# Performance work log

Measured on AMD Instinct MI355X. Metric: run time of the kernel, lower is better.

Reference implementation:

```python
import jax, jax.numpy as jnp
import numpy as np

EMBED = 128
NUM_HOPS = 3
VOCAB = 32000
MEM = 50
PAD = 0


def pos_weights(J, d):
    # MemN2N position encoding: 1 - (j+1)/J - (k+1)/d * (1 - 2*(j+1)/J)
    j = jnp.arange(J, dtype=jnp.float32)[:, None]
    k = jnp.arange(d, dtype=jnp.float32)[None, :]
    return 1.0 - (j + 1.0) / J - (k + 1.0) / d * (1.0 - 2.0 * (j + 1.0) / J)


def setup_inputs() -> dict:
    key = jax.random.key(0)
    ks = jax.random.split(key, 10)
    ctx_query = jax.random.randint(ks[0], (16, 10, 20), 0, VOCAB)
    story = jax.random.randint(ks[1], (16, MEM, 40), 0, VOCAB)

    def emb(k):
        w = 0.1 * jax.random.normal(k, (VOCAB, EMBED), dtype=jnp.float32)
        return w.at[PAD].set(0.0)  # padding_idx row is zero

    A_w = emb(ks[2])
    C_w = emb(ks[3])
    B_w = emb(ks[4])
    H_w = 0.1 * jax.random.normal(ks[5], (EMBED, EMBED), dtype=jnp.float32)
    H_b = 0.1 * jax.random.normal(ks[6], (EMBED,), dtype=jnp.float32)
    out_w = 0.1 * jax.random.normal(ks[7], (VOCAB, EMBED), dtype=jnp.float32)
    TA = 0.1 * jax.random.normal(ks[8], (MEM, EMBED), dtype=jnp.float32)
    TC = 0.1 * jax.random.normal(ks[9], (MEM, EMBED), dtype=jnp.float32)
    return {"ctx_query": ctx_query, "story": story, "A_w": A_w, "C_w": C_w,
            "B_w": B_w, "H_w": H_w, "H_b": H_b, "out_w": out_w, "TA": TA, "TC": TC}


def reference(ctx_query, story, A_w, C_w, B_w, H_w, H_b, out_w, TA, TC):
    B, NQ, S = ctx_query.shape
    R, S2 = story.shape[1], story.shape[2]
    cq = ctx_query.reshape(B * NQ, S)
    # story repeated across num_qa (broadcast instead of materialized repeat)
    st = jnp.broadcast_to(story[:, None], (B, NQ, R, S2)).reshape(B * NQ, R, S2)

    qw = pos_weights(S, EMBED)            # [S, d]
    state = jnp.sum(B_w[cq] * qw, axis=1)  # [BN, d]

    sw = pos_weights(S2, EMBED)           # [S2, d]
    for _ in range(NUM_HOPS):             # use_lw=True: A/C tied across hops
        mem = jnp.sum(A_w[st] * sw, axis=2) + TA    # [BN, R, d]
        outm = jnp.sum(C_w[st] * sw, axis=2) + TC   # [BN, R, d]
        probs = jax.nn.softmax(jnp.einsum('brd,bd->br', mem, state), axis=-1)
        response = jnp.einsum('br,brd->bd', probs, outm)  # [BN, d]
        state = response @ H_w.T + H_b + state      # H(response) + state
    return state @ out_w.T                          # [BN, vocab]
```

## Files before the change

kernel.cpp:

```cpp
#include <hip/hip_runtime.h>
#include <hip/hip_bf16.h>
#include <math.h>

#define EMBED 128
#define VOCAB 32000
#define MEMN  50
#define BATCH 16
#define NQ    10
#define SQ    20
#define SS    40
#define BN    (BATCH*NQ)
#define NHOPS 3
#define NV    64

typedef short v8s __attribute__((ext_vector_type(8)));
typedef float v4f __attribute__((ext_vector_type(4)));

__device__ __forceinline__ float posw(int j, int J, int k) {
    float jf = (float)(j + 1) / (float)J;
    return 1.0f - jf - ((float)(k + 1) / (float)EMBED) * (1.0f - 2.0f * jf);
}

__device__ __forceinline__ short f2bf(float f) {
    __hip_bfloat16 h = __float2bfloat16(f);
    return *(short*)&h;
}

__global__ void k_embed(const int* __restrict__ cq, const int* __restrict__ story,
                        const float* __restrict__ Bw, const float* __restrict__ Aw,
                        const float* __restrict__ Cw, const float* __restrict__ TA,
                        const float* __restrict__ TC, const float* __restrict__ Hw,
                        float* __restrict__ state, float* __restrict__ memb,
                        float* __restrict__ outb, float* __restrict__ HwT) {
    int blk = blockIdx.x;
    int t = threadIdx.x;
    if (blk < BN) {
        float acc = 0.f;
        #pragma unroll
        for (int s = 0; s < SQ; ++s) {
            int tok = cq[blk * SQ + s];
            acc += Bw[tok * EMBED + t] * posw(s, SQ, t);
        }
        state[blk * EMBED + t] = acc;
    } else if (blk < BN + BATCH * MEMN) {
        int br = blk - BN;
        int r = br % MEMN;
        float ma = TA[r * EMBED + t];
        float mc = TC[r * EMBED + t];
        const int* toks = story + br * SS;
        #pragma unroll 4
        for (int s = 0; s < SS; ++s) {
            int tok = toks[s];
            float w = posw(s, SS, t);
            ma += Aw[tok * EMBED + t] * w;
            mc += Cw[tok * EMBED + t] * w;
        }
        memb[br * EMBED + t] = ma;
        outb[br * EMBED + t] = mc;
    } else {
        int k = blk - (BN + BATCH * MEMN);
        HwT[k * EMBED + t] = Hw[t * EMBED + k];
    }
}

__global__ void k_hops(const float* __restrict__ memb, const float* __restrict__ outb,
                       const float* __restrict__ HwT, const float* __restrict__ Hb,
                       const float* __restrict__ state, __hip_bfloat16* __restrict__ stateb) {
    __shared__ float lmem[MEMN][EMBED + 1];
    __shared__ float lout[MEMN][EMBED + 1];
    __shared__ float lstate[EMBED];
    __shared__ float lprobs[MEMN];
    __shared__ float lresp[EMBED];
    int bn = blockIdx.x;
    int b  = bn / NQ;
    int t  = threadIdx.x;
    for (int i = t; i < MEMN * EMBED; i += EMBED) {
        int r = i >> 7, d = i & 127;
        lmem[r][d] = memb[b * MEMN * EMBED + i];
        lout[r][d] = outb[b * MEMN * EMBED + i];
    }
    lstate[t] = state[bn * EMBED + t];
    __syncthreads();

    for (int hop = 0; hop < NHOPS; ++hop) {
        float logit = -1e30f;
        if (t < MEMN) {
            float acc = 0.f;
            for (int d = 0; d < EMBED; ++d) acc += lmem[t][d] * lstate[d];
            logit = acc;
        }
        if (t < 64) {
            float m = logit;
            #pragma unroll
            for (int off = 32; off; off >>= 1) m = fmaxf(m, __shfl_xor(m, off, 64));
            float e = (t < MEMN) ? __expf(logit - m) : 0.f;
            float ssum = e;
            #pragma unroll
            for (int off = 32; off; off >>= 1) ssum += __shfl_xor(ssum, off, 64);
            if (t < MEMN) lprobs[t] = e / ssum;
        }
        __syncthreads();
        float resp = 0.f;
        for (int r = 0; r < MEMN; ++r) resp += lprobs[r] * lout[r][t];
        lresp[t] = resp;
        __syncthreads();
        float acc = Hb[t] + lstate[t];
        for (int k = 0; k < EMBED; ++k) acc += lresp[k] * HwT[k * EMBED + t];
        __syncthreads();
        lstate[t] = acc;
        __syncthreads();
    }
    stateb[bn * EMBED + t] = __float2bfloat16(lstate[t]);
}

__global__ __launch_bounds__(256) void k_out(const __hip_bfloat16* __restrict__ stateb,
                                             const float* __restrict__ outw,
                                             float* __restrict__ out) {
    __shared__ __align__(16) __hip_bfloat16 Alds[BN][EMBED + 8];
    __shared__ __align__(16) __hip_bfloat16 Blds[NV][EMBED + 8];
    int t = threadIdx.x;
    int vbase = blockIdx.x * NV;

    #pragma unroll
    for (int i = 0; i < 10; ++i) {
        int e = t + i * 256;
        int row = e >> 4, c8 = (e & 15) << 3;
        *(int4*)&Alds[row][c8] = *(const int4*)&stateb[row * EMBED + c8];
    }
    #pragma unroll
    for (int i = 0; i < 8; ++i) {
        int e = t + i * 256;
        int row = e >> 5, c4 = (e & 31) << 2;
        float4 w = *(const float4*)&outw[(size_t)(vbase + row) * EMBED + c4];
        short4 p;
        p.x = f2bf(w.x); p.y = f2bf(w.y); p.z = f2bf(w.z); p.w = f2bf(w.w);
        *(short4*)&Blds[row][c4] = p;
    }
    __syncthreads();

    int wv = t >> 6;
    int l = t & 63;
    int col16 = l & 15;
    int kg = l >> 4;

    v8s bfrag[4];
    #pragma unroll
    for (int k4 = 0; k4 < 4; ++k4)
        bfrag[k4] = *(v8s*)&Blds[(wv << 4) + col16][k4 * 32 + kg * 8];

    v4f acc[10];
    #pragma unroll
    for (int m = 0; m < 10; ++m) acc[m] = (v4f){0.f, 0.f, 0.f, 0.f};

    #pragma unroll
    for (int k4 = 0; k4 < 4; ++k4) {
        #pragma unroll
        for (int m = 0; m < 10; ++m) {
            v8s af = *(v8s*)&Alds[m * 16 + col16][k4 * 32 + kg * 8];
            acc[m] = __builtin_amdgcn_mfma_f32_16x16x32_bf16(af, bfrag[k4], acc[m], 0, 0, 0);
        }
    }

    int colg = vbase + (wv << 4) + col16;
    #pragma unroll
    for (int m = 0; m < 10; ++m) {
        #pragma unroll
        for (int i = 0; i < 4; ++i) {
            out[(size_t)(m * 16 + kg * 4 + i) * VOCAB + colg] = acc[m][i];
        }
    }
}

extern "C" void kernel_launch(void* const* d_in, const int* in_sizes, int n_in,
                              void* d_out, int out_size, void* d_ws, size_t ws_size,
                              hipStream_t stream) {
    const int*   ctx_query = (const int*)  d_in[0];
    const int*   story     = (const int*)  d_in[1];
    const float* A_w       = (const float*)d_in[2];
    const float* C_w       = (const float*)d_in[3];
    const float* B_w       = (const float*)d_in[4];
    const float* H_w       = (const float*)d_in[5];
    const float* H_b       = (const float*)d_in[6];
    const float* out_w     = (const float*)d_in[7];
    const float* TA        = (const float*)d_in[8];
    const float* TC        = (const float*)d_in[9];
    float* out = (float*)d_out;

    float* ws    = (float*)d_ws;
    float* state = ws;
    float* memb  = state + BN * EMBED;
    float* outb  = memb + BATCH * MEMN * EMBED;
    float* HwT   = outb + BATCH * MEMN * EMBED;
    __hip_bfloat16* stateb = (__hip_bfloat16*)(HwT + EMBED * EMBED);

    k_embed<<<BN + BATCH * MEMN + EMBED, EMBED, 0, stream>>>(
        ctx_query, story, B_w, A_w, C_w, TA, TC, H_w, state, memb, outb, HwT);
    k_hops<<<BN, EMBED, 0, stream>>>(memb, outb, HwT, H_b, state, stateb);
    k_out<<<VOCAB / NV, 256, 0, stream>>>(stateb, out_w, out);
}
```

Before: 35.39 us.

## Restructure embedding gather into float4 loads split across token groups

The embedding kernel now stages token ids in shared memory and has each thread load float4 slices of embedding rows. The 128 threads are split into 4 groups over token positions, and partial sums are reduced through shared memory. Position weights are computed with hoisted per-token coefficients. This aims to raise memory-level parallelism and cut serial dependent gathers per thread, at the cost of extra syncs and a reduction step. The hop kernel loops also get unroll pragmas.

```diff
diff --git a/kernel.cpp b/kernel.cpp
--- a/kernel.cpp
+++ b/kernel.cpp
@@ -16,11 +16,6 @@
 typedef short v8s __attribute__((ext_vector_type(8)));
 typedef float v4f __attribute__((ext_vector_type(4)));
 
-__device__ __forceinline__ float posw(int j, int J, int k) {
-    float jf = (float)(j + 1) / (float)J;
-    return 1.0f - jf - ((float)(k + 1) / (float)EMBED) * (1.0f - 2.0f * jf);
-}
-
 __device__ __forceinline__ short f2bf(float f) {
     __hip_bfloat16 h = __float2bfloat16(f);
     return *(short*)&h;
@@ -32,31 +27,90 @@
                         const float* __restrict__ TC, const float* __restrict__ Hw,
                         float* __restrict__ state, float* __restrict__ memb,
                         float* __restrict__ outb, float* __restrict__ HwT) {
+    __shared__ int ltok[SS];
+    __shared__ float4 redA[4][32];
+    __shared__ float4 redC[4][32];
     int blk = blockIdx.x;
     int t = threadIdx.x;
+    int sg = t >> 5;
+    int d4 = t & 31;
+    int k0 = d4 << 2;
+
     if (blk < BN) {
-        float acc = 0.f;
-        #pragma unroll
-        for (int s = 0; s < SQ; ++s) {
-            int tok = cq[blk * SQ + s];
-            acc += Bw[tok * EMBED + t] * posw(s, SQ, t);
-        }
-        state[blk * EMBED + t] = acc;
+        int bn = blk;
+        if (t < SQ) ltok[t] = cq[bn * SQ + t];
+        __syncthreads();
+        float4 acc = {0.f, 0.f, 0.f, 0.f};
+        #pragma unroll
+        for (int i = 0; i < SQ / 4; ++i) {
+            int s = sg + (i << 2);
+            int tok = ltok[s];
+            float jf = (float)(s + 1) * (1.0f / SQ);
+            float c0 = 1.0f - jf;
+            float c1 = (1.0f - 2.0f * jf) * (1.0f / EMBED);
+            float4 a = *(const float4*)&Bw[(size_t)tok * EMBED + k0];
+            acc.x += a.x * (c0 - (float)(k0 + 1) * c1);
+            acc.y += a.y * (c0 - (float)(k0 + 2) * c1);
+            acc.z += a.z * (c0 - (float)(k0 + 3) * c1);
+            acc.w += a.w * (c0 - (float)(k0 + 4) * c1);
+        }
+        redA[sg][d4] = acc;
+        __syncthreads();
+        if (t < 32) {
+            float4 s0 = redA[0][t], s1 = redA[1][t], s2 = redA[2][t], s3 = redA[3][t];
+            float4 o;
+            o.x = s0.x + s1.x + s2.x + s3.x;
+            o.y = s0.y + s1.y + s2.y + s3.y;
+            o.z = s0.z + s1.z + s2.z + s3.z;
+            o.w = s0.w + s1.w + s2.w + s3.w;
+            *(float4*)&state[bn * EMBED + (t << 2)] = o;
+        }
     } else if (blk < BN + BATCH * MEMN) {
         int br = blk - BN;
         int r = br % MEMN;
-        float ma = TA[r * EMBED + t];
-        float mc = TC[r * EMBED + t];
-        const int* toks = story + br * SS;
-        #pragma unroll 4
-        for (int s = 0; s < SS; ++s) {
-            int tok = toks[s];
-            float w = posw(s, SS, t);
-            ma += Aw[tok * EMBED + t] * w;
-            mc += Cw[tok * EMBED + t] * w;
-        }
-        memb[br * EMBED + t] = ma;
-        outb[br * EMBED + t] = mc;
+        if (t < SS) ltok[t] = story[br * SS + t];
+        __syncthreads();
+        float4 accA = {0.f, 0.f, 0.f, 0.f};
+        float4 accC = {0.f, 0.f, 0.f, 0.f};
+        #pragma unroll
+        for (int i = 0; i < SS / 4; ++i) {
+            int s = sg + (i << 2);
+            int tok = ltok[s];
+            float jf = (float)(s + 1) * (1.0f / SS);
+            float c0 = 1.0f - jf;
+            float c1 = (1.0f - 2.0f * jf) * (1.0f / EMBED);
+            float w0 = c0 - (float)(k0 + 1) * c1;
+            float w1 = c0 - (float)(k0 + 2) * c1;
+            float w2 = c0 - (float)(k0 + 3) * c1;
+            float w3 = c0 - (float)(k0 + 4) * c1;
+            float4 a = *(const float4*)&Aw[(size_t)tok * EMBED + k0];
+            float4 c = *(const float4*)&Cw[(size_t)tok * EMBED + k0];
+            accA.x += a.x * w0; accA.y += a.y * w1; accA.z += a.z * w2; accA.w += a.w * w3;
+            accC.x += c.x * w0; accC.y += c.y * w1; accC.z += c.z * w2; accC.w += c.w * w3;
+        }
+        redA[sg][d4] = accA;
+        redC[sg][d4] = accC;
+        __syncthreads();
+        if (t < 32) {
+            float4 s0 = redA[0][t], s1 = redA[1][t], s2 = redA[2][t], s3 = redA[3][t];
+            float4 ta = *(const float4*)&TA[r * EMBED + (t << 2)];
+            float4 o;
+            o.x = s0.x + s1.x + s2.x + s3.x + ta.x;
+            o.y = s0.y + s1.y + s2.y + s3.y + ta.y;
+            o.z = s0.z + s1.z + s2.z + s3.z + ta.z;
+            o.w = s0.w + s1.w + s2.w + s3.w + ta.w;
+            *(float4*)&memb[br * EMBED + (t << 2)] = o;
+        } else if (t < 64) {
+            int u = t - 32;
+            float4 s0 = redC[0][u], s1 = redC[1][u], s2 = redC[2][u], s3 = redC[3][u];
+            float4 tc = *(const float4*)&TC[r * EMBED + (u << 2)];
+            float4 o;
+            o.x = s0.x + s1.x + s2.x + s3.x + tc.x;
+            o.y = s0.y + s1.y + s2.y + s3.y + tc.y;
+            o.z = s0.z + s1.z + s2.z + s3.z + tc.z;
+            o.w = s0.w + s1.w + s2.w + s3.w + tc.w;
+            *(float4*)&outb[br * EMBED + (u << 2)] = o;
+        }
     } else {
         int k = blk - (BN + BATCH * MEMN);
         HwT[k * EMBED + t] = Hw[t * EMBED + k];
@@ -86,6 +140,7 @@
         float logit = -1e30f;
         if (t < MEMN) {
             float acc = 0.f;
+            #pragma unroll 8
             for (int d = 0; d < EMBED; ++d) acc += lmem[t][d] * lstate[d];
             logit = acc;
         }
@@ -101,10 +156,12 @@
         }
         __syncthreads();
         float resp = 0.f;
+        #pragma unroll 10
         for (int r = 0; r < MEMN; ++r) resp += lprobs[r] * lout[r][t];
         lresp[t] = resp;
         __syncthreads();
         float acc = Hb[t] + lstate[t];
+        #pragma unroll 8
         for (int k = 0; k < EMBED; ++k) acc += lresp[k] * HwT[k * EMBED + t];
         __syncthreads();
         lstate[t] = acc;
@@ -193,7 +250,7 @@
     float* HwT   = outb + BATCH * MEMN * EMBED;
     __hip_bfloat16* stateb = (__hip_bfloat16*)(HwT + EMBED * EMBED);
 
-    k_embed<<<BN + BATCH * MEMN + EMBED, EMBED, 0, stream>>>(
+    k_embed<<<BN + BATCH * MEMN + EMBED, 128, 0, stream>>>(
         ctx_query, story, B_w, A_w, C_w, TA, TC, H_w, state, memb, outb, HwT);
     k_hops<<<BN, EMBED, 0, stream>>>(memb, outb, HwT, H_b, state, stateb);
     k_out<<<VOCAB / NV, 256, 0, stream>>>(stateb, out_w, out);
```

Result: slower. 39.06 us (+10.3%).

## Store state in MFMA fragment layout and drop LDS staging in output GEMM

Applied to the files above, without the earlier changes.

The hop kernel now writes the final bf16 state directly in a fragment-major layout, so the output projection can load MFMA A-operands straight from global memory with contiguous 16-byte loads. The output kernel drops its shared-memory staging and the block barrier. It now runs one 64-thread wave per 16 vocab columns and loads out_w fragments directly into registers. This removes LDS traffic and synchronisation, but it launches four times as many blocks and each wave re-reads the state from L2 rather than sharing it across a block.

```diff
diff --git a/kernel.cpp b/kernel.cpp
--- a/kernel.cpp
+++ b/kernel.cpp
@@ -11,7 +11,6 @@
 #define SS    40
 #define BN    (BATCH*NQ)
 #define NHOPS 3
-#define NV    64
 
 typedef short v8s __attribute__((ext_vector_type(8)));
 typedef float v4f __attribute__((ext_vector_type(4)));
@@ -65,7 +64,7 @@
 
 __global__ void k_hops(const float* __restrict__ memb, const float* __restrict__ outb,
                        const float* __restrict__ HwT, const float* __restrict__ Hb,
-                       const float* __restrict__ state, __hip_bfloat16* __restrict__ stateb) {
+                       const float* __restrict__ state, __hip_bfloat16* __restrict__ stateF) {
     __shared__ float lmem[MEMN][EMBED + 1];
     __shared__ float lout[MEMN][EMBED + 1];
     __shared__ float lstate[EMBED];
@@ -110,64 +109,51 @@
         lstate[t] = acc;
         __syncthreads();
     }
-    stateb[bn * EMBED + t] = __float2bfloat16(lstate[t]);
+    int frag = ((t >> 5) << 2) | ((t >> 3) & 3);
+    stateF[((size_t)frag * BN + bn) * 8 + (t & 7)] = __float2bfloat16(lstate[t]);
 }
 
-__global__ __launch_bounds__(256) void k_out(const __hip_bfloat16* __restrict__ stateb,
-                                             const float* __restrict__ outw,
-                                             float* __restrict__ out) {
-    __shared__ __align__(16) __hip_bfloat16 Alds[BN][EMBED + 8];
-    __shared__ __align__(16) __hip_bfloat16 Blds[NV][EMBED + 8];
-    int t = threadIdx.x;
-    int vbase = blockIdx.x * NV;
-
-    #pragma unroll
-    for (int i = 0; i < 10; ++i) {
-        int e = t + i * 256;
-        int row = e >> 4, c8 = (e & 15) << 3;
-        *(int4*)&Alds[row][c8] = *(const int4*)&stateb[row * EMBED + c8];
-    }
-    #pragma unroll
-    for (int i = 0; i < 8; ++i) {
-        int e = t + i * 256;
-        int row = e >> 5, c4 = (e & 31) << 2;
-        float4 w = *(const float4*)&outw[(size_t)(vbase + row) * EMBED + c4];
-        short4 p;
-        p.x = f2bf(w.x); p.y = f2bf(w.y); p.z = f2bf(w.z); p.w = f2bf(w.w);
-        *(short4*)&Blds[row][c4] = p;
-    }
-    __syncthreads();
-
-    int wv = t >> 6;
-    int l = t & 63;
+__global__ __launch_bounds__(64) void k_out(const __hip_bfloat16* __restrict__ stateF,
+                                            const float* __restrict__ outw,
+                                            float* __restrict__ out) {
+    int l = threadIdx.x;
     int col16 = l & 15;
     int kg = l >> 4;
+    int vbase = blockIdx.x << 4;
+    int v = vbase + col16;
 
     v8s bfrag[4];
     #pragma unroll
-    for (int k4 = 0; k4 < 4; ++k4)
-        bfrag[k4] = *(v8s*)&Blds[(wv << 4) + col16][k4 * 32 + kg * 8];
+    for (int k4 = 0; k4 < 4; ++k4) {
+        const float4* p = (const float4*)&outw[(size_t)v * EMBED + k4 * 32 + kg * 8];
+        float4 w0 = p[0], w1 = p[1];
+        v8s bf;
+        bf[0] = f2bf(w0.x); bf[1] = f2bf(w0.y); bf[2] = f2bf(w0.z); bf[3] = f2bf(w0.w);
+        bf[4] = f2bf(w1.x); bf[5] = f2bf(w1.y); bf[6] = f2bf(w1.z); bf[7] = f2bf(w1.w);
+        bfrag[k4] = bf;
+    }
 
     v4f acc[10];
     #pragma unroll
     for (int m = 0; m < 10; ++m) acc[m] = (v4f){0.f, 0.f, 0.f, 0.f};
 
+    const v8s* aF = (const v8s*)stateF;
     #pragma unroll
     for (int k4 = 0; k4 < 4; ++k4) {
+        v8s af[10];
         #pragma unroll
-        for (int m = 0; m < 10; ++m) {
-            v8s af = *(v8s*)&Alds[m * 16 + col16][k4 * 32 + kg * 8];
-            acc[m] = __builtin_amdgcn_mfma_f32_16x16x32_bf16(af, bfrag[k4], acc[m], 0, 0, 0);
-        }
+        for (int m = 0; m < 10; ++m)
+            af[m] = aF[(((k4 << 2) | kg) * BN) + m * 16 + col16];
+        #pragma unroll
+        for (int m = 0; m < 10; ++m)
+            acc[m] = __builtin_amdgcn_mfma_f32_16x16x32_bf16(af[m], bfrag[k4], acc[m], 0, 0, 0);
     }
 
-    int colg = vbase + (wv << 4) + col16;
     #pragma unroll
     for (int m = 0; m < 10; ++m) {
         #pragma unroll
-        for (int i = 0; i < 4; ++i) {
-            out[(size_t)(m * 16 + kg * 4 + i) * VOCAB + colg] = acc[m][i];
-        }
+        for (int i = 0; i < 4; ++i)
+            out[(size_t)(m * 16 + kg * 4 + i) * VOCAB + v] = acc[m][i];
     }
 }
 
@@ -191,10 +177,10 @@
     float* memb  = state + BN * EMBED;
     float* outb  = memb + BATCH * MEMN * EMBED;
     float* HwT   = outb + BATCH * MEMN * EMBED;
-    __hip_bfloat16* stateb = (__hip_bfloat16*)(HwT + EMBED * EMBED);
+    __hip_bfloat16* stateF = (__hip_bfloat16*)(HwT + EMBED * EMBED);
 
     k_embed<<<BN + BATCH * MEMN + EMBED, EMBED, 0, stream>>>(
         ctx_query, story, B_w, A_w, C_w, TA, TC, H_w, state, memb, outb, HwT);
-    k_hops<<<BN, EMBED, 0, stream>>>(memb, outb, HwT, H_b, state, stateb);
-    k_out<<<VOCAB / NV, 256, 0, stream>>>(stateb, out_w, out);
+    k_hops<<<BN, EMBED, 0, stream>>>(memb, outb, HwT, H_b, state, stateF);
+    k_out<<<VOCAB / 16, 64, 0, stream>>>(stateF, out_w, out);
 }
```

After: 36.78 us. 3.9% more time.

## Run hop kernel as single wavefront without barriers, swizzled LDS, vectorized loads

Applied to the files above, without the earlier changes.

Restructures the hop kernel to use one 64-lane wavefront per query, so every __syncthreads is removed and only compiler memory fences remain, each lane handling two embedding dimensions. The memory tiles are loaded with float4 into an XOR-swizzled LDS layout to avoid bank conflicts without padding, and the H matrix is read directly as rows with float4 loads instead of through the transposed copy. The risks are fewer threads per block, which lowers parallelism during the load phase, and correctness depending on wavefront lockstep semantics for LDS visibility.

```diff
diff --git a/kernel.cpp b/kernel.cpp
--- a/kernel.cpp
+++ b/kernel.cpp
@@ -63,54 +63,86 @@
     }
 }
 
-__global__ void k_hops(const float* __restrict__ memb, const float* __restrict__ outb,
-                       const float* __restrict__ HwT, const float* __restrict__ Hb,
-                       const float* __restrict__ state, __hip_bfloat16* __restrict__ stateb) {
-    __shared__ float lmem[MEMN][EMBED + 1];
-    __shared__ float lout[MEMN][EMBED + 1];
+__global__ __launch_bounds__(64) void k_hops(const float* __restrict__ memb,
+                                             const float* __restrict__ outb,
+                                             const float* __restrict__ Hw,
+                                             const float* __restrict__ Hb,
+                                             const float* __restrict__ state,
+                                             __hip_bfloat16* __restrict__ stateb) {
+    __shared__ float lmem[MEMN][EMBED];
+    __shared__ float lout[MEMN][EMBED];
     __shared__ float lstate[EMBED];
     __shared__ float lprobs[MEMN];
     __shared__ float lresp[EMBED];
     int bn = blockIdx.x;
     int b  = bn / NQ;
-    int t  = threadIdx.x;
-    for (int i = t; i < MEMN * EMBED; i += EMBED) {
-        int r = i >> 7, d = i & 127;
-        lmem[r][d] = memb[b * MEMN * EMBED + i];
-        lout[r][d] = outb[b * MEMN * EMBED + i];
-    }
-    lstate[t] = state[bn * EMBED + t];
-    __syncthreads();
-
+    int l  = threadIdx.x;
+    int d0 = l, d1 = l + 64;
+
+    size_t base = (size_t)b * MEMN * EMBED;
+    #pragma unroll 5
+    for (int i = l; i < MEMN * EMBED / 4; i += 64) {
+        int row = i >> 5, c4 = i & 31;
+        int sc4 = c4 ^ (row & 7);
+        *(float4*)&lmem[row][sc4 << 2] = *(const float4*)&memb[base + ((size_t)i << 2)];
+        *(float4*)&lout[row][sc4 << 2] = *(const float4*)&outb[base + ((size_t)i << 2)];
+    }
+    float st0 = state[bn * EMBED + d0];
+    float st1 = state[bn * EMBED + d1];
+    lstate[d0] = st0; lstate[d1] = st1;
+    float hb0 = Hb[d0], hb1 = Hb[d1];
+    asm volatile("" ::: "memory");
+
+    int r = (l < MEMN) ? l : 0;
     for (int hop = 0; hop < NHOPS; ++hop) {
-        float logit = -1e30f;
-        if (t < MEMN) {
-            float acc = 0.f;
-            for (int d = 0; d < EMBED; ++d) acc += lmem[t][d] * lstate[d];
-            logit = acc;
-        }
-        if (t < 64) {
-            float m = logit;
-            #pragma unroll
-            for (int off = 32; off; off >>= 1) m = fmaxf(m, __shfl_xor(m, off, 64));
-            float e = (t < MEMN) ? __expf(logit - m) : 0.f;
-            float ssum = e;
-            #pragma unroll
-            for (int off = 32; off; off >>= 1) ssum += __shfl_xor(ssum, off, 64);
-            if (t < MEMN) lprobs[t] = e / ssum;
-        }
-        __syncthreads();
-        float resp = 0.f;
-        for (int r = 0; r < MEMN; ++r) resp += lprobs[r] * lout[r][t];
-        lresp[t] = resp;
-        __syncthreads();
-        float acc = Hb[t] + lstate[t];
-        for (int k = 0; k < EMBED; ++k) acc += lresp[k] * HwT[k * EMBED + t];
-        __syncthreads();
-        lstate[t] = acc;
-        __syncthreads();
-    }
-    stateb[bn * EMBED + t] = __float2bfloat16(lstate[t]);
+        float a0 = 0.f, a1 = 0.f, a2 = 0.f, a3 = 0.f;
+        #pragma unroll
+        for (int j = 0; j < 32; ++j) {
+            float4 m = *(const float4*)&lmem[r][(j ^ (r & 7)) << 2];
+            float4 s = *(const float4*)&lstate[j << 2];
+            a0 += m.x * s.x; a1 += m.y * s.y; a2 += m.z * s.z; a3 += m.w * s.w;
+        }
+        float logit = (l < MEMN) ? (a0 + a1) + (a2 + a3) : -1e30f;
+        float mx = logit;
+        #pragma unroll
+        for (int off = 32; off; off >>= 1) mx = fmaxf(mx, __shfl_xor(mx, off, 64));
+        float e = (l < MEMN) ? __expf(logit - mx) : 0.f;
+        float ss = e;
+        #pragma unroll
+        for (int off = 32; off; off >>= 1) ss += __shfl_xor(ss, off, 64);
+        if (l < MEMN) lprobs[l] = e / ss;
+        asm volatile("" ::: "memory");
+        float r0 = 0.f, r1 = 0.f, q0 = 0.f, q1 = 0.f;
+        #pragma unroll
+        for (int k = 0; k < MEMN; k += 2) {
+            float p0 = lprobs[k], p1 = lprobs[k + 1];
+            r0 += p0 * lout[k    ][(((d0 >> 2) ^ (k & 7)) << 2)       | (d0 & 3)];
+            q0 += p0 * lout[k    ][(((d1 >> 2) ^ (k & 7)) << 2)       | (d1 & 3)];
+            r1 += p1 * lout[k + 1][(((d0 >> 2) ^ ((k + 1) & 7)) << 2) | (d0 & 3)];
+            q1 += p1 * lout[k + 1][(((d1 >> 2) ^ ((k + 1) & 7)) << 2) | (d1 & 3)];
+        }
+        lresp[d0] = r0 + r1;
+        lresp[d1] = q0 + q1;
+        asm volatile("" ::: "memory");
+        float h00 = hb0 + st0, h01 = 0.f, h02 = 0.f, h03 = 0.f;
+        float h10 = hb1 + st1, h11 = 0.f, h12 = 0.f, h13 = 0.f;
+        #pragma unroll 8
+        for (int j = 0; j < 32; ++j) {
+            float4 rv = *(const float4*)&lresp[j << 2];
+            float4 w0 = *(const float4*)&Hw[(size_t)d0 * EMBED + (j << 2)];
+            float4 w1 = *(const float4*)&Hw[(size_t)d1 * EMBED + (j << 2)];
+            h00 += rv.x * w0.x; h01 += rv.y * w0.y; h02 += rv.z * w0.z; h03 += rv.w * w0.w;
+            h10 += rv.x * w1.x; h11 += rv.y * w1.y; h12 += rv.z * w1.z; h13 += rv.w * w1.w;
+        }
+        st0 = (h00 + h01) + (h02 + h03);
+        st1 = (h10 + h11) + (h12 + h13);
+        if (hop < NHOPS - 1) {
+            lstate[d0] = st0; lstate[d1] = st1;
+            asm volatile("" ::: "memory");
+        }
+    }
+    stateb[bn * EMBED + d0] = __float2bfloat16(st0);
+    stateb[bn * EMBED + d1] = __float2bfloat16(st1);
 }
 
 __global__ __launch_bounds__(256) void k_out(const __hip_bfloat16* __restrict__ stateb,
@@ -195,6 +227,6 @@
 
     k_embed<<<BN + BATCH * MEMN + EMBED, EMBED, 0, stream>>>(
         ctx_query, story, B_w, A_w, C_w, TA, TC, H_w, state, memb, outb, HwT);
-    k_hops<<<BN, EMBED, 0, stream>>>(memb, outb, HwT, H_b, state, stateb);
+    k_hops<<<BN, 64, 0, stream>>>(memb, outb, H_w, H_b, state, stateb);
     k_out<<<VOCAB / NV, 256, 0, stream>>>(stateb, out_w, out);
 }
```

Measured after the change: 36.24 us. 1.02x slower.
